# Kernel tuning notes

Measured on AMD Instinct MI355X. Metric: run time of the kernel, lower is better.

Reference implementation:

```python
import jax, jax.numpy as jnp
import numpy as np

B, N, M, DIN, H = 8, 2048, 2048, 512, 256
SCALE = float(np.sqrt(H))


def _lin_params(key, din, dout):
    kw, kb = jax.random.split(key)
    lim = 1.0 / np.sqrt(din)
    W = jax.random.uniform(kw, (din, dout), jnp.float32, -lim, lim)
    b = jax.random.uniform(kb, (dout,), jnp.float32, -lim, lim)
    return W, b


def setup_inputs() -> dict:
    key = jax.random.key(0)
    ks = jax.random.split(key, 16)
    inp = {
        "q_fp": jax.random.normal(ks[0], (B, N, DIN), jnp.float32),
        "v_ret": jax.random.normal(ks[1], (B, M, DIN), jnp.float32),
        "pi_star": jax.random.uniform(ks[2], (B, N, M), jnp.float32),
    }
    names = ["qs", "ks", "vs", "qe", "ke", "ve"]
    for i, nm in enumerate(names):
        W, b = _lin_params(ks[3 + i], DIN, H)
        inp[f"W{nm}"], inp[f"b{nm}"] = W, b
    inp["W1"], inp["b1"] = _lin_params(ks[10], 4 * H, H)
    inp["W2"], inp["b2"] = _lin_params(ks[11], H, H)
    inp["gamma"] = jnp.ones((1,), jnp.float32)
    inp["ew"] = jnp.array(1.0, jnp.float32)
    return inp


def _forward(q_fp, v_ret, pi_star, Wqs, bqs, Wks, bks, Wvs, bvs,
             Wqe, bqe, Wke, bke, Wve, bve, W1, b1, W2, b2, gamma, ew):
    q_struct = q_fp @ Wqs + bqs          # [B,N,H]
    k_struct = v_ret @ Wks + bks         # [B,M,H]
    v_struct = v_ret @ Wvs + bvs
    q_elec = q_fp @ Wqe + bqe
    k_elec = v_ret @ Wke + bke
    v_elec = v_ret @ Wve + bve

    structural_logits = jnp.einsum("bnh,bmh->bnm", q_struct, k_struct) / SCALE

    # cdist(p=2) via the quadratic expansion, clamped for numeric safety
    q2 = jnp.sum(q_elec * q_elec, -1, keepdims=True)          # [B,N,1]
    k2 = jnp.sum(k_elec * k_elec, -1, keepdims=True)          # [B,M,1]
    d2 = q2 + jnp.swapaxes(k2, -2, -1) - 2.0 * jnp.einsum("bnh,bmh->bnm", q_elec, k_elec)
    electronic_distance = jnp.sqrt(jnp.maximum(d2, 1e-12))    # [B,N,M]
    electronic_scale = jnp.maximum(
        electronic_distance.mean(axis=(-2, -1), keepdims=True), 1e-4)
    electronic_logits = -(electronic_distance / electronic_scale)

    pi_mask = gamma * jnp.log(jnp.maximum(pi_star, 1e-9))
    final_logits = structural_logits + ew * electronic_logits + pi_mask
    attn = jax.nn.softmax(final_logits, axis=-1)              # [B,N,M]

    ctx_s = jnp.einsum("bnm,bmh->bnh", attn, v_struct)
    ctx_e = jnp.einsum("bnm,bmh->bnh", attn, v_elec)
    fused = jnp.concatenate([ctx_s, ctx_e, ctx_s - ctx_e, ctx_s * ctx_e], axis=-1)
    h = jax.nn.silu(fused @ W1 + b1)
    return h @ W2 + b2


def reference(q_fp, v_ret, pi_star, Wqs, bqs, Wks, bks, Wvs, bvs,
              Wqe, bqe, Wke, bke, Wve, bve, W1, b1, W2, b2, gamma, ew):
    return _forward(q_fp, v_ret, pi_star, Wqs, bqs, Wks, bks, Wvs, bvs,
                    Wqe, bqe, Wke, bke, Wve, bve, W1, b1, W2, b2, gamma, ew)
```

## Files before the change

### kernel.cpp

```cpp
#include <hip/hip_runtime.h>

#define Bsz 8
#define Nq  2048
#define Mk  2048
#define BKt 32

typedef __attribute__((ext_vector_type(8))) short   short8;
typedef __attribute__((ext_vector_type(4))) float   floatx4;

__device__ __forceinline__ unsigned short f2bf(float f) {
  union { float f; unsigned u; } x; x.f = f;
  unsigned r = x.u + 0x7fffu + ((x.u >> 16) & 1u);
  return (unsigned short)(r >> 16);
}
__device__ __forceinline__ float bf2f(unsigned short s) {
  union { unsigned u; float f; } x; x.u = ((unsigned)s) << 16;
  return x.f;
}

__device__ __forceinline__ void gemm_core_nt(
    const unsigned short* __restrict__ A, int lda,
    const unsigned short* __restrict__ B, int ldb,
    int K, unsigned short* ldsA, unsigned short* ldsB,
    floatx4 (&acc)[4][4])
{
  const int tid  = threadIdx.x;
  const int lane = tid & 63;
  const int sr   = tid >> 2;
  const int sc   = (tid & 3) << 3;
  const int wid  = tid >> 6;
  const int wm   = wid & 1;
  const int wn   = wid >> 1;
  const int fr   = lane & 15;
  const int fk   = (lane >> 4) << 3;

  const unsigned short* a0p = A + (size_t)sr * lda + sc;
  const unsigned short* a1p = A + (size_t)(sr + 64) * lda + sc;
  const unsigned short* b0p = B + (size_t)sr * ldb + sc;
  const unsigned short* b1p = B + (size_t)(sr + 64) * ldb + sc;
  uint4* sa0 = (uint4*)(ldsA + sr * BKt + sc);
  uint4* sa1 = (uint4*)(ldsA + (sr + 64) * BKt + sc);
  uint4* sb0 = (uint4*)(ldsB + sr * BKt + sc);
  uint4* sb1 = (uint4*)(ldsB + (sr + 64) * BKt + sc);
  const unsigned short* fa = ldsA + (wm * 64 + fr) * BKt + fk;
  const unsigned short* fb = ldsB + (wn * 64 + fr) * BKt + fk;

  for (int k0 = 0; k0 < K; k0 += BKt) {
    uint4 a0 = *(const uint4*)a0p; a0p += BKt;
    uint4 a1 = *(const uint4*)a1p; a1p += BKt;
    uint4 b0 = *(const uint4*)b0p; b0p += BKt;
    uint4 b1 = *(const uint4*)b1p; b1p += BKt;
    __syncthreads();
    *sa0 = a0; *sa1 = a1; *sb0 = b0; *sb1 = b1;
    __syncthreads();
    short8 af[4], bfr[4];
#pragma unroll
    for (int i = 0; i < 4; i++) af[i]  = *(const short8*)(fa + i * 16 * BKt);
#pragma unroll
    for (int i = 0; i < 4; i++) bfr[i] = *(const short8*)(fb + i * 16 * BKt);
#pragma unroll
    for (int i = 0; i < 4; i++)
#pragma unroll
      for (int j = 0; j < 4; j++)
        acc[i][j] = __builtin_amdgcn_mfma_f32_16x16x32_bf16(af[i], bfr[j], acc[i][j], 0, 0, 0);
  }
}

__device__ __forceinline__ void gemm_core_nt64(
    const unsigned short* __restrict__ A, int lda,
    const unsigned short* __restrict__ B, int ldb,
    int K, unsigned short* ldsA, unsigned short* ldsB,
    floatx4 (&acc)[4][2])
{
  const int tid  = threadIdx.x;
  const int lane = tid & 63;
  const int sr   = tid >> 2;
  const int sc   = (tid & 3) << 3;
  const int wid  = tid >> 6;
  const int wm   = wid & 1;
  const int wn   = wid >> 1;
  const int fr   = lane & 15;
  const int fk   = (lane >> 4) << 3;

  const unsigned short* a0p = A + (size_t)sr * lda + sc;
  const unsigned short* a1p = A + (size_t)(sr + 64) * lda + sc;
  const unsigned short* bp  = B + (size_t)sr * ldb + sc;
  uint4* sa0 = (uint4*)(ldsA + sr * BKt + sc);
  uint4* sa1 = (uint4*)(ldsA + (sr + 64) * BKt + sc);
  uint4* sb  = (uint4*)(ldsB + sr * BKt + sc);
  const unsigned short* fa = ldsA + (wm * 64 + fr) * BKt + fk;
  const unsigned short* fb = ldsB + (wn * 32 + fr) * BKt + fk;

  for (int k0 = 0; k0 < K; k0 += BKt) {
    uint4 a0 = *(const uint4*)a0p; a0p += BKt;
    uint4 a1 = *(const uint4*)a1p; a1p += BKt;
    uint4 b0 = *(const uint4*)bp;  bp  += BKt;
    __syncthreads();
    *sa0 = a0; *sa1 = a1; *sb = b0;
    __syncthreads();
    short8 af[4], bfr[2];
#pragma unroll
    for (int i = 0; i < 4; i++) af[i]  = *(const short8*)(fa + i * 16 * BKt);
#pragma unroll
    for (int j = 0; j < 2; j++) bfr[j] = *(const short8*)(fb + j * 16 * BKt);
#pragma unroll
    for (int i = 0; i < 4; i++)
#pragma unroll
      for (int j = 0; j < 2; j++)
        acc[i][j] = __builtin_amdgcn_mfma_f32_16x16x32_bf16(af[i], bfr[j], acc[i][j], 0, 0, 0);
  }
}

#define EPILOGUE_VARS \
  const int lane = threadIdx.x & 63; \
  const int wid  = threadIdx.x >> 6; \
  const int wm   = wid & 1; \
  const int wn   = wid >> 1; \
  const int r4   = (lane >> 4) * 4;  \
  const int cn   = lane & 15; \
  (void)wid;

__global__ __launch_bounds__(256, 2) void k_proj(
    const float* __restrict__ A, const unsigned short* __restrict__ Bw,
    const float* __restrict__ bias, unsigned short* __restrict__ Cout,
    int Ncols, int K)
{
  __shared__ alignas(16) unsigned short ldsA[128 * BKt];
  __shared__ alignas(16) unsigned short ldsB[128 * BKt];
  floatx4 acc[4][4];
#pragma unroll
  for (int i = 0; i < 4; i++)
#pragma unroll
    for (int j = 0; j < 4; j++)
#pragma unroll
      for (int t = 0; t < 4; t++) acc[i][j][t] = 0.f;

  const int tid = threadIdx.x;
  const int ar  = tid >> 1;
  const int ac  = (tid & 1) << 4;
  const int sr  = tid >> 2;
  const int sc  = (tid & 3) << 3;

  const float* ap = A + ((size_t)blockIdx.x * 128 + ar) * K + ac;
  const unsigned short* b0p = Bw + ((size_t)blockIdx.y * 128 + sr) * K + sc;
  const unsigned short* b1p = b0p + (size_t)64 * K;
  uint4* sa  = (uint4*)(ldsA + ar * BKt + ac);
  uint4* sb0 = (uint4*)(ldsB + sr * BKt + sc);
  uint4* sb1 = (uint4*)(ldsB + (sr + 64) * BKt + sc);

  {
    const int lane = tid & 63;
    const int wm   = (tid >> 6) & 1;
    const int wn   = tid >> 7;
    const int fr   = lane & 15;
    const int fk   = (lane >> 4) << 3;
    const unsigned short* fa = ldsA + (wm * 64 + fr) * BKt + fk;
    const unsigned short* fb = ldsB + (wn * 64 + fr) * BKt + fk;

    for (int k0 = 0; k0 < K; k0 += BKt) {
      float4 f0 = *(const float4*)(ap + 0);
      float4 f1 = *(const float4*)(ap + 4);
      float4 f2 = *(const float4*)(ap + 8);
      float4 f3 = *(const float4*)(ap + 12);
      ap += BKt;
      uint4 b0 = *(const uint4*)b0p; b0p += BKt;
      uint4 b1 = *(const uint4*)b1p; b1p += BKt;
      uint4 pa, pb;
      pa.x = f2bf(f0.x) | ((unsigned)f2bf(f0.y) << 16);
      pa.y = f2bf(f0.z) | ((unsigned)f2bf(f0.w) << 16);
      pa.z = f2bf(f1.x) | ((unsigned)f2bf(f1.y) << 16);
      pa.w = f2bf(f1.z) | ((unsigned)f2bf(f1.w) << 16);
      pb.x = f2bf(f2.x) | ((unsigned)f2bf(f2.y) << 16);
      pb.y = f2bf(f2.z) | ((unsigned)f2bf(f2.w) << 16);
      pb.z = f2bf(f3.x) | ((unsigned)f2bf(f3.y) << 16);
      pb.w = f2bf(f3.z) | ((unsigned)f2bf(f3.w) << 16);
      __syncthreads();
      sa[0] = pa; sa[1] = pb;
      *sb0 = b0; *sb1 = b1;
      __syncthreads();
      short8 af[4], bfr[4];
#pragma unroll
      for (int i = 0; i < 4; i++) af[i]  = *(const short8*)(fa + i * 16 * BKt);
#pragma unroll
      for (int i = 0; i < 4; i++) bfr[i] = *(const short8*)(fb + i * 16 * BKt);
#pragma unroll
      for (int i = 0; i < 4; i++)
#pragma unroll
        for (int j = 0; j < 4; j++)
          acc[i][j] = __builtin_amdgcn_mfma_f32_16x16x32_bf16(af[i], bfr[j], acc[i][j], 0, 0, 0);
    }
  }

  EPILOGUE_VARS
#pragma unroll
  for (int i = 0; i < 4; i++) {
#pragma unroll
    for (int j = 0; j < 4; j++) {
      int gc = blockIdx.y * 128 + wn * 64 + j * 16 + cn;
      float bv = bias[gc];
#pragma unroll
      for (int r = 0; r < 4; r++) {
        int gr = blockIdx.x * 128 + wm * 64 + i * 16 + r4 + r;
        Cout[(size_t)gr * Ncols + gc] = f2bf(acc[i][j][r] + bv);
      }
    }
  }
}

template<int MODE>
__global__ __launch_bounds__(256, 3) void k_gemm_bias(
    const unsigned short* __restrict__ A, const unsigned short* __restrict__ Bw,
    const float* __restrict__ bias, void* __restrict__ Cout, int Ncols, int K)
{
  __shared__ alignas(16) unsigned short ldsA[128 * BKt];
  __shared__ alignas(16) unsigned short ldsB[128 * BKt];
  floatx4 acc[4][4];
#pragma unroll
  for (int i = 0; i < 4; i++)
#pragma unroll
    for (int j = 0; j < 4; j++)
#pragma unroll
      for (int t = 0; t < 4; t++) acc[i][j][t] = 0.f;

  const unsigned short* Ab = A + (size_t)blockIdx.x * 128 * K;
  const unsigned short* Bb = Bw + (size_t)blockIdx.y * 128 * K;
  gemm_core_nt(Ab, K, Bb, K, K, ldsA, ldsB, acc);

  EPILOGUE_VARS
#pragma unroll
  for (int i = 0; i < 4; i++) {
#pragma unroll
    for (int j = 0; j < 4; j++) {
      int gc = blockIdx.y * 128 + wn * 64 + j * 16 + cn;
      float bv = bias[gc];
#pragma unroll
      for (int r = 0; r < 4; r++) {
        int gr = blockIdx.x * 128 + wm * 64 + i * 16 + r4 + r;
        float v = acc[i][j][r] + bv;
        if constexpr (MODE == 1) v = v / (1.f + __expf(-v));
        if constexpr (MODE == 2)
          ((float*)Cout)[(size_t)gr * Ncols + gc] = v;
        else
          ((unsigned short*)Cout)[(size_t)gr * Ncols + gc] = f2bf(v);
      }
    }
  }
}

__global__ __launch_bounds__(256, 3) void k_pass1(
    const unsigned short* __restrict__ Xq, const unsigned short* __restrict__ Xk,
    const float* __restrict__ q2, const float* __restrict__ k2,
    float* __restrict__ dsum, float* __restrict__ rowsum)
{
  {
    int blin = (blockIdx.z * 16 + blockIdx.y) * 16 + blockIdx.x;
    if (threadIdx.x < 8) rowsum[blin * 8 + threadIdx.x] = 0.f;
  }
  __shared__ alignas(16) unsigned short ldsA[128 * BKt];
  __shared__ alignas(16) unsigned short ldsB[128 * BKt];
  floatx4 acc[4][4];
#pragma unroll
  for (int i = 0; i < 4; i++)
#pragma unroll
    for (int j = 0; j < 4; j++)
#pragma unroll
      for (int t = 0; t < 4; t++) acc[i][j][t] = 0.f;

  const int b = blockIdx.z;
  const unsigned short* Ab = Xq + ((size_t)(b * Nq) + blockIdx.x * 128) * 512 + 256;
  const unsigned short* Bb = Xk + ((size_t)(b * Mk) + blockIdx.y * 128) * 1024 + 512;
  gemm_core_nt(Ab, 512, Bb, 1024, 256, ldsA, ldsB, acc);

  EPILOGUE_VARS
  const int rowBase = b * Nq + blockIdx.x * 128;
  const int colBase = b * Mk + blockIdx.y * 128;
  float lsum = 0.f;
#pragma unroll
  for (int i = 0; i < 4; i++) {
#pragma unroll
    for (int j = 0; j < 4; j++) {
      float kk = k2[colBase + wn * 64 + j * 16 + cn];
#pragma unroll
      for (int r = 0; r < 4; r++) {
        float qq = q2[rowBase + wm * 64 + i * 16 + r4 + r];
        lsum += sqrtf(fmaxf(qq + kk - 2.f * acc[i][j][r], 1e-12f));
      }
    }
  }
#pragma unroll
  for (int o = 32; o; o >>= 1) lsum += __shfl_down(lsum, o);
  __syncthreads();
  float* red = (float*)ldsA;
  if (lane == 0) red[wid] = lsum;
  __syncthreads();
  if (threadIdx.x == 0) atomicAdd(dsum + b, red[0] + red[1] + red[2] + red[3]);
}

__global__ __launch_bounds__(256, 3) void k_logits(
    const unsigned short* __restrict__ Xq, const unsigned short* __restrict__ Xk,
    const float* __restrict__ q2, const float* __restrict__ k2,
    const float* __restrict__ dsum, const float* __restrict__ pi,
    const float* __restrict__ gamma_p, const float* __restrict__ ew_p,
    unsigned short* __restrict__ attn, float* __restrict__ rowsum)
{
  __shared__ alignas(16) unsigned short ldsA[128 * BKt];
  __shared__ alignas(16) unsigned short ldsB[64 * BKt];
  floatx4 accS[4][2], accE[4][2];
#pragma unroll
  for (int i = 0; i < 4; i++)
#pragma unroll
    for (int j = 0; j < 2; j++)
#pragma unroll
      for (int t = 0; t < 4; t++) { accS[i][j][t] = 0.f; accE[i][j][t] = 0.f; }

  const int b = blockIdx.z;
  const unsigned short* Aq_s = Xq + ((size_t)(b * Nq) + blockIdx.x * 128) * 512;
  const unsigned short* Bk_s = Xk + ((size_t)(b * Mk) + blockIdx.y * 64) * 1024;
  gemm_core_nt64(Aq_s,       512, Bk_s,       1024, 256, ldsA, ldsB, accS);
  gemm_core_nt64(Aq_s + 256, 512, Bk_s + 512, 1024, 256, ldsA, ldsB, accE);

  const float scale = fmaxf(dsum[b] * (1.f / (2048.f * 2048.f)), 1e-4f);
  const float einv  = ew_p[0] / scale;
  const float gv    = gamma_p[0];
  const bool  g1    = (gv == 1.0f);

  EPILOGUE_VARS
#pragma unroll
  for (int i = 0; i < 4; i++) {
    float rs4[4] = {0.f, 0.f, 0.f, 0.f};
#pragma unroll
    for (int j = 0; j < 2; j++) {
      int m = blockIdx.y * 64 + wn * 32 + j * 16 + cn;
      float kk = k2[b * Mk + m];
#pragma unroll
      for (int r = 0; r < 4; r++) {
        int n = blockIdx.x * 128 + wm * 64 + i * 16 + r4 + r;
        float qq = q2[b * Nq + n];
        size_t idx = ((size_t)b * Nq + n) * Mk + m;
        float d  = sqrtf(fmaxf(qq + kk - 2.f * accE[i][j][r], 1e-12f));
        float p  = fmaxf(pi[idx], 1e-9f);
        float pf = g1 ? p : __expf(gv * __logf(p));
        float e  = __expf(accS[i][j][r] * 0.0625f - einv * d) * pf;
        rs4[r] += e;
        attn[idx] = f2bf(e);
      }
    }
#pragma unroll
    for (int r = 0; r < 4; r++) {
      float v = rs4[r];
      v += __shfl_xor(v, 1); v += __shfl_xor(v, 2);
      v += __shfl_xor(v, 4); v += __shfl_xor(v, 8);
      if (cn == 0)
        atomicAdd(rowsum + b * Nq + blockIdx.x * 128 + wm * 64 + i * 16 + r4 + r, v);
    }
  }
}

__global__ __launch_bounds__(256, 3) void k_pv(
    const unsigned short* __restrict__ At, const unsigned short* __restrict__ VT,
    const float* __restrict__ rowsum, unsigned short* __restrict__ ctx)
{
  __shared__ alignas(16) unsigned short ldsA[128 * BKt];
  __shared__ alignas(16) unsigned short ldsB[64 * BKt];
  floatx4 acc[4][2];
#pragma unroll
  for (int i = 0; i < 4; i++)
#pragma unroll
    for (int j = 0; j < 2; j++)
#pragma unroll
      for (int t = 0; t < 4; t++) acc[i][j][t] = 0.f;

  const int b = blockIdx.z;
  const unsigned short* Ab = At + ((size_t)b * Nq + blockIdx.x * 128) * (size_t)Mk;
  const unsigned short* Bb = VT + ((size_t)b * 512 + blockIdx.y * 64) * (size_t)Mk;
  gemm_core_nt64(Ab, Mk, Bb, Mk, Mk, ldsA, ldsB, acc);

  EPILOGUE_VARS
  const int rowbase = b * Nq + blockIdx.x * 128 + wm * 64;
#pragma unroll
  for (int i = 0; i < 4; i++) {
    float rinv[4];
#pragma unroll
    for (int r = 0; r < 4; r++)
      rinv[r] = 1.f / rowsum[rowbase + i * 16 + r4 + r];
#pragma unroll
    for (int j = 0; j < 2; j++) {
      int gc = blockIdx.y * 64 + wn * 32 + j * 16 + cn;
#pragma unroll
      for (int r = 0; r < 4; r++) {
        int gr = blockIdx.x * 128 + wm * 64 + i * 16 + r4 + r;
        ctx[((size_t)b * Nq + gr) * 512 + gc] = f2bf(acc[i][j][r] * rinv[r]);
      }
    }
  }
}

__global__ void k_prep_w(
    const float* __restrict__ Wqs, const float* __restrict__ Wqe,
    const float* __restrict__ Wks, const float* __restrict__ Wvs,
    const float* __restrict__ Wke, const float* __restrict__ Wve,
    const float* __restrict__ W1,  const float* __restrict__ W2,
    const float* __restrict__ bqs, const float* __restrict__ bqe,
    const float* __restrict__ bks, const float* __restrict__ bvs,
    const float* __restrict__ bke, const float* __restrict__ bve,
    unsigned short* __restrict__ WqT, unsigned short* __restrict__ WkT,
    unsigned short* __restrict__ W1T, unsigned short* __restrict__ W2T,
    float* __restrict__ bq, float* __restrict__ bk, float* __restrict__ dsum)
{
  int gid = blockIdx.x * 256 + threadIdx.x;
  int idx = gid;
  if (idx < 512 * 512) {
    int j = idx >> 9, k = idx & 511;
    float v = (j < 256) ? Wqs[k * 256 + j] : Wqe[k * 256 + (j - 256)];
    WqT[idx] = f2bf(v);
  } else if ((idx -= 512 * 512) < 1024 * 512) {
    int j = idx >> 9, k = idx & 511;
    int s = j >> 8, jj = j & 255;
    const float* Wp = (s == 0) ? Wks : (s == 1) ? Wvs : (s == 2) ? Wke : Wve;
    WkT[idx] = f2bf(Wp[k * 256 + jj]);
  } else if ((idx -= 1024 * 512) < 256 * 1024) {
    int j = idx >> 10, k = idx & 1023;
    W1T[idx] = f2bf(W1[k * 256 + j]);
  } else if ((idx -= 256 * 1024) < 256 * 256) {
    int j = idx >> 8, k = idx & 255;
    W2T[idx] = f2bf(W2[k * 256 + j]);
  }
  if (gid < 512)  bq[gid] = (gid < 256) ? bqs[gid] : bqe[gid - 256];
  if (gid < 1024) bk[gid] = (gid < 256) ? bks[gid]
                    : (gid < 512) ? bvs[gid - 256]
                    : (gid < 768) ? bke[gid - 512] : bve[gid - 768];
  if (gid < 8) dsum[gid] = 0.f;
}

__global__ __launch_bounds__(256) void k_rowsq(
    const unsigned short* __restrict__ X, int stride, int colOff, float* __restrict__ out)
{
  int row = blockIdx.x * 4 + (threadIdx.x >> 6);
  int lane = threadIdx.x & 63;
  const unsigned short* p = X + (size_t)row * stride + colOff + lane * 4;
  uint2 u = *(const uint2*)p;
  float a0 = bf2f((unsigned short)(u.x & 0xffff));
  float a1 = bf2f((unsigned short)(u.x >> 16));
  float a2 = bf2f((unsigned short)(u.y & 0xffff));
  float a3 = bf2f((unsigned short)(u.y >> 16));
  float s = a0 * a0 + a1 * a1 + a2 * a2 + a3 * a3;
#pragma unroll
  for (int o = 32; o; o >>= 1) s += __shfl_down(s, o);
  if (lane == 0) out[row] = s;
}

__global__ void k_trans_vt(const unsigned short* __restrict__ Xk, unsigned short* __restrict__ VT) {
  __shared__ unsigned short t[32][33];
  const int b = blockIdx.z;
  const int m0 = blockIdx.x * 32, j0 = blockIdx.y * 32;
  const int tx = threadIdx.x, ty = threadIdx.y;
#pragma unroll
  for (int i = 0; i < 4; i++) {
    int m = m0 + ty + i * 8;
    int j = j0 + tx;
    int c = (j < 256) ? (256 + j) : (512 + j);
    t[ty + i * 8][tx] = Xk[((size_t)b * Mk + m) * 1024 + c];
  }
  __syncthreads();
#pragma unroll
  for (int i = 0; i < 4; i++) {
    int j = j0 + ty + i * 8;
    int m = m0 + tx;
    VT[((size_t)b * 512 + j) * Mk + m] = t[tx][ty + i * 8];
  }
}

__global__ void k_fused(const unsigned short* __restrict__ ctx, unsigned short* __restrict__ fused) {
  int idx = blockIdx.x * 256 + threadIdx.x;
  int bn = idx >> 8;
  int j = idx & 255;
  float cs = bf2f(ctx[(size_t)bn * 512 + j]);
  float ce = bf2f(ctx[(size_t)bn * 512 + 256 + j]);
  size_t o = (size_t)bn * 1024 + j;
  fused[o]       = f2bf(cs);
  fused[o + 256] = f2bf(ce);
  fused[o + 512] = f2bf(cs - ce);
  fused[o + 768] = f2bf(cs * ce);
}

extern "C" void kernel_launch(void* const* d_in, const int* in_sizes, int n_in,
                              void* d_out, int out_size, void* d_ws, size_t ws_size,
                              hipStream_t stream) {
  (void)in_sizes; (void)n_in; (void)out_size; (void)ws_size;
  const float* q_fp  = (const float*)d_in[0];
  const float* v_ret = (const float*)d_in[1];
  const float* pi    = (const float*)d_in[2];
  const float* Wqs = (const float*)d_in[3];  const float* bqs = (const float*)d_in[4];
  const float* Wks = (const float*)d_in[5];  const float* bks = (const float*)d_in[6];
  const float* Wvs = (const float*)d_in[7];  const float* bvs = (const float*)d_in[8];
  const float* Wqe = (const float*)d_in[9];  const float* bqe = (const float*)d_in[10];
  const float* Wke = (const float*)d_in[11]; const float* bke = (const float*)d_in[12];
  const float* Wve = (const float*)d_in[13]; const float* bve = (const float*)d_in[14];
  const float* W1  = (const float*)d_in[15]; const float* b1  = (const float*)d_in[16];
  const float* W2  = (const float*)d_in[17]; const float* b2  = (const float*)d_in[18];
  const float* gamma = (const float*)d_in[19];
  const float* ew    = (const float*)d_in[20];

  char* w = (char*)d_ws;
  unsigned short* WqT = (unsigned short*)(w + 0);
  unsigned short* WkT = (unsigned short*)(w + 524288);
  unsigned short* W1T = (unsigned short*)(w + 1572864);
  unsigned short* W2T = (unsigned short*)(w + 2097152);
  float* bq   = (float*)(w + 2228224);
  float* bk   = (float*)(w + 2230272);
  float* q2   = (float*)(w + 2234368);
  float* k2   = (float*)(w + 2299904);
  float* dsum = (float*)(w + 2365440);
  unsigned short* ctx  = (unsigned short*)(w + 2365696);
  unsigned short* hbuf = (unsigned short*)(w + 19142912);
  unsigned short* Xq = (unsigned short*)(w + 35920128);
  unsigned short* Xk = (unsigned short*)(w + 52697344);
  unsigned short* VT = (unsigned short*)(w + 86251776);
  unsigned short* attn = (unsigned short*)(w + 103028992);
  unsigned short* fused = attn;
  float* rowsum = (float*)d_out;

  k_prep_w<<<4352, 256, 0, stream>>>(Wqs, Wqe, Wks, Wvs, Wke, Wve, W1, W2,
                                     bqs, bqe, bks, bvs, bke, bve,
                                     WqT, WkT, W1T, W2T, bq, bk, dsum);
  k_proj<<<dim3(128, 4), 256, 0, stream>>>(q_fp,  WqT, bq, Xq, 512, 512);
  k_proj<<<dim3(128, 8), 256, 0, stream>>>(v_ret, WkT, bk, Xk, 1024, 512);
  k_rowsq<<<4096, 256, 0, stream>>>(Xq, 512, 256, q2);
  k_rowsq<<<4096, 256, 0, stream>>>(Xk, 1024, 512, k2);
  k_pass1<<<dim3(16, 16, 8), 256, 0, stream>>>(Xq, Xk, q2, k2, dsum, rowsum);
  k_logits<<<dim3(16, 32, 8), 256, 0, stream>>>(Xq, Xk, q2, k2, dsum, pi, gamma, ew,
                                                attn, rowsum);
  k_trans_vt<<<dim3(64, 16, 8), dim3(32, 8), 0, stream>>>(Xk, VT);
  k_pv<<<dim3(16, 8, 8), 256, 0, stream>>>(attn, VT, rowsum, ctx);
  k_fused<<<16384, 256, 0, stream>>>(ctx, fused);
  k_gemm_bias<1><<<dim3(128, 2), 256, 0, stream>>>(fused, W1T, b1, hbuf, 256, 1024);
  k_gemm_bias<2><<<dim3(128, 2), 256, 0, stream>>>(hbuf, W2T, b2, d_out, 256, 256);
}
```

Measured before the change: 583.5 us.

## Compute score GEMMs once, stash packed bf16 logits, then row-wise softmax pass

The distance-only first pass and the logits kernel that recomputed both GEMMs are merged into one kernel, k_sd. It computes the structural and electronic GEMMs once, accumulates the distance mean, and writes the scaled structural score and the distance as packed bf16 pairs into a scratch buffer. A new row-oriented kernel then reads that buffer together with pi using coalesced vector loads, applies the exp and mask, writes attn, and produces rowsum directly without atomics. The work runs in four chunks of two batches so the 32MB scratch buffer reuses the ctx/hbuf region and may stay cache-resident. The trade-off is extra global traffic for the intermediate buffer and bf16 rounding of the logit components before the exp.

```diff
diff --git a/kernel.cpp b/kernel.cpp
--- a/kernel.cpp
+++ b/kernel.cpp
@@ -247,43 +247,49 @@
   }
 }
 
-__global__ __launch_bounds__(256, 3) void k_pass1(
+__global__ __launch_bounds__(256, 2) void k_sd(
     const unsigned short* __restrict__ Xq, const unsigned short* __restrict__ Xk,
     const float* __restrict__ q2, const float* __restrict__ k2,
-    float* __restrict__ dsum, float* __restrict__ rowsum)
-{
-  {
-    int blin = (blockIdx.z * 16 + blockIdx.y) * 16 + blockIdx.x;
-    if (threadIdx.x < 8) rowsum[blin * 8 + threadIdx.x] = 0.f;
-  }
+    int b0, float* __restrict__ dsum, unsigned* __restrict__ sd)
+{
   __shared__ alignas(16) unsigned short ldsA[128 * BKt];
   __shared__ alignas(16) unsigned short ldsB[128 * BKt];
-  floatx4 acc[4][4];
+  floatx4 accS[4][4], accE[4][4];
 #pragma unroll
   for (int i = 0; i < 4; i++)
 #pragma unroll
     for (int j = 0; j < 4; j++)
 #pragma unroll
-      for (int t = 0; t < 4; t++) acc[i][j][t] = 0.f;
-
-  const int b = blockIdx.z;
-  const unsigned short* Ab = Xq + ((size_t)(b * Nq) + blockIdx.x * 128) * 512 + 256;
-  const unsigned short* Bb = Xk + ((size_t)(b * Mk) + blockIdx.y * 128) * 1024 + 512;
-  gemm_core_nt(Ab, 512, Bb, 1024, 256, ldsA, ldsB, acc);
+      for (int t = 0; t < 4; t++) { accS[i][j][t] = 0.f; accE[i][j][t] = 0.f; }
+
+  const int z = blockIdx.z;
+  const int b = b0 + z;
+  const unsigned short* Aq = Xq + ((size_t)(b * Nq) + blockIdx.x * 128) * 512;
+  const unsigned short* Bk = Xk + ((size_t)(b * Mk) + blockIdx.y * 128) * 1024;
+  gemm_core_nt(Aq,       512, Bk,       1024, 256, ldsA, ldsB, accS);
+  gemm_core_nt(Aq + 256, 512, Bk + 512, 1024, 256, ldsA, ldsB, accE);
 
   EPILOGUE_VARS
-  const int rowBase = b * Nq + blockIdx.x * 128;
-  const int colBase = b * Mk + blockIdx.y * 128;
+  float kkv[4];
+#pragma unroll
+  for (int j = 0; j < 4; j++)
+    kkv[j] = k2[b * Mk + blockIdx.y * 128 + wn * 64 + j * 16 + cn];
+
   float lsum = 0.f;
 #pragma unroll
   for (int i = 0; i < 4; i++) {
 #pragma unroll
-    for (int j = 0; j < 4; j++) {
-      float kk = k2[colBase + wn * 64 + j * 16 + cn];
-#pragma unroll
-      for (int r = 0; r < 4; r++) {
-        float qq = q2[rowBase + wm * 64 + i * 16 + r4 + r];
-        lsum += sqrtf(fmaxf(qq + kk - 2.f * acc[i][j][r], 1e-12f));
+    for (int r = 0; r < 4; r++) {
+      const int n = blockIdx.x * 128 + wm * 64 + i * 16 + r4 + r;
+      const float qq = q2[b * Nq + n];
+      unsigned* srow = sd + (size_t)(z * Nq + n) * Mk;
+#pragma unroll
+      for (int j = 0; j < 4; j++) {
+        const int m = blockIdx.y * 128 + wn * 64 + j * 16 + cn;
+        float d = sqrtf(fmaxf(qq + kkv[j] - 2.f * accE[i][j][r], 1e-12f));
+        lsum += d;
+        srow[m] = (unsigned)f2bf(accS[i][j][r] * 0.0625f)
+                | ((unsigned)f2bf(d) << 16);
       }
     }
   }
@@ -296,64 +302,53 @@
   if (threadIdx.x == 0) atomicAdd(dsum + b, red[0] + red[1] + red[2] + red[3]);
 }
 
-__global__ __launch_bounds__(256, 3) void k_logits(
-    const unsigned short* __restrict__ Xq, const unsigned short* __restrict__ Xk,
-    const float* __restrict__ q2, const float* __restrict__ k2,
-    const float* __restrict__ dsum, const float* __restrict__ pi,
-    const float* __restrict__ gamma_p, const float* __restrict__ ew_p,
+__global__ __launch_bounds__(256) void k_softmax(
+    const unsigned* __restrict__ sd, const float* __restrict__ pi,
+    const float* __restrict__ dsum, const float* __restrict__ gamma_p,
+    const float* __restrict__ ew_p, int b0,
     unsigned short* __restrict__ attn, float* __restrict__ rowsum)
 {
-  __shared__ alignas(16) unsigned short ldsA[128 * BKt];
-  __shared__ alignas(16) unsigned short ldsB[64 * BKt];
-  floatx4 accS[4][2], accE[4][2];
-#pragma unroll
-  for (int i = 0; i < 4; i++)
-#pragma unroll
-    for (int j = 0; j < 2; j++)
-#pragma unroll
-      for (int t = 0; t < 4; t++) { accS[i][j][t] = 0.f; accE[i][j][t] = 0.f; }
-
-  const int b = blockIdx.z;
-  const unsigned short* Aq_s = Xq + ((size_t)(b * Nq) + blockIdx.x * 128) * 512;
-  const unsigned short* Bk_s = Xk + ((size_t)(b * Mk) + blockIdx.y * 64) * 1024;
-  gemm_core_nt64(Aq_s,       512, Bk_s,       1024, 256, ldsA, ldsB, accS);
-  gemm_core_nt64(Aq_s + 256, 512, Bk_s + 512, 1024, 256, ldsA, ldsB, accE);
+  const int wid  = threadIdx.x >> 6;
+  const int lane = threadIdx.x & 63;
+  const int rl   = blockIdx.x * 4 + wid;
+  const int b    = b0 + (rl >> 11);
+  const int n    = rl & 2047;
 
   const float scale = fmaxf(dsum[b] * (1.f / (2048.f * 2048.f)), 1e-4f);
   const float einv  = ew_p[0] / scale;
   const float gv    = gamma_p[0];
   const bool  g1    = (gv == 1.0f);
 
-  EPILOGUE_VARS
-#pragma unroll
-  for (int i = 0; i < 4; i++) {
-    float rs4[4] = {0.f, 0.f, 0.f, 0.f};
-#pragma unroll
-    for (int j = 0; j < 2; j++) {
-      int m = blockIdx.y * 64 + wn * 32 + j * 16 + cn;
-      float kk = k2[b * Mk + m];
-#pragma unroll
-      for (int r = 0; r < 4; r++) {
-        int n = blockIdx.x * 128 + wm * 64 + i * 16 + r4 + r;
-        float qq = q2[b * Nq + n];
-        size_t idx = ((size_t)b * Nq + n) * Mk + m;
-        float d  = sqrtf(fmaxf(qq + kk - 2.f * accE[i][j][r], 1e-12f));
-        float p  = fmaxf(pi[idx], 1e-9f);
-        float pf = g1 ? p : __expf(gv * __logf(p));
-        float e  = __expf(accS[i][j][r] * 0.0625f - einv * d) * pf;
-        rs4[r] += e;
-        attn[idx] = f2bf(e);
-      }
+  const unsigned*  sp = sd  + (size_t)rl * Mk;
+  const float*     pp = pi  + ((size_t)b * Nq + n) * Mk;
+  unsigned short*  ap = attn + ((size_t)b * Nq + n) * Mk;
+
+  float rs = 0.f;
+  for (int it = 0; it < 8; ++it) {
+    const int c = it * 256 + lane * 4;
+    const uint4  sv = *(const uint4*)(sp + c);
+    const float4 pv = *(const float4*)(pp + c);
+    const unsigned uu[4]  = {sv.x, sv.y, sv.z, sv.w};
+    const float    pp4[4] = {pv.x, pv.y, pv.z, pv.w};
+    float e[4];
+#pragma unroll
+    for (int t = 0; t < 4; ++t) {
+      union { unsigned u; float f; } cs, cd;
+      cs.u = uu[t] << 16;
+      cd.u = uu[t] & 0xffff0000u;
+      float p  = fmaxf(pp4[t], 1e-9f);
+      float pf = g1 ? p : __expf(gv * __logf(p));
+      e[t] = __expf(cs.f - einv * cd.f) * pf;
+      rs += e[t];
     }
-#pragma unroll
-    for (int r = 0; r < 4; r++) {
-      float v = rs4[r];
-      v += __shfl_xor(v, 1); v += __shfl_xor(v, 2);
-      v += __shfl_xor(v, 4); v += __shfl_xor(v, 8);
-      if (cn == 0)
-        atomicAdd(rowsum + b * Nq + blockIdx.x * 128 + wm * 64 + i * 16 + r4 + r, v);
-    }
-  }
+    uint2 st;
+    st.x = (unsigned)f2bf(e[0]) | ((unsigned)f2bf(e[1]) << 16);
+    st.y = (unsigned)f2bf(e[2]) | ((unsigned)f2bf(e[3]) << 16);
+    *(uint2*)(ap + c) = st;
+  }
+#pragma unroll
+  for (int o = 32; o; o >>= 1) rs += __shfl_down(rs, o);
+  if (lane == 0) rowsum[b * Nq + n] = rs;
 }
 
 __global__ __launch_bounds__(256, 3) void k_pv(
@@ -518,6 +513,7 @@
   unsigned short* VT = (unsigned short*)(w + 86251776);
   unsigned short* attn = (unsigned short*)(w + 103028992);
   unsigned short* fused = attn;
+  unsigned* sdbuf = (unsigned*)(w + 2365696);
   float* rowsum = (float*)d_out;
 
   k_prep_w<<<4352, 256, 0, stream>>>(Wqs, Wqe, Wks, Wvs, Wke, Wve, W1, W2,
@@ -527,9 +523,11 @@
   k_proj<<<dim3(128, 8), 256, 0, stream>>>(v_ret, WkT, bk, Xk, 1024, 512);
   k_rowsq<<<4096, 256, 0, stream>>>(Xq, 512, 256, q2);
   k_rowsq<<<4096, 256, 0, stream>>>(Xk, 1024, 512, k2);
-  k_pass1<<<dim3(16, 16, 8), 256, 0, stream>>>(Xq, Xk, q2, k2, dsum, rowsum);
-  k_logits<<<dim3(16, 32, 8), 256, 0, stream>>>(Xq, Xk, q2, k2, dsum, pi, gamma, ew,
-                                                attn, rowsum);
+  for (int c = 0; c < 4; ++c) {
+    k_sd<<<dim3(16, 16, 2), 256, 0, stream>>>(Xq, Xk, q2, k2, 2 * c, dsum, sdbuf);
+    k_softmax<<<1024, 256, 0, stream>>>(sdbuf, pi, dsum, gamma, ew, 2 * c,
+                                        attn, rowsum);
+  }
   k_trans_vt<<<dim3(64, 16, 8), dim3(32, 8), 0, stream>>>(Xk, VT);
   k_pv<<<dim3(16, 8, 8), 256, 0, stream>>>(attn, VT, rowsum, ctx);
   k_fused<<<16384, 256, 0, stream>>>(ctx, fused);
```

Result: no change. 580.4 us (-0.5%).
